# Kernel optimization log

Hardware: AMD Instinct MI355X
Metric: run time of the kernel (lower is better)

The kernel has to match this reference:

```python
import jax, jax.numpy as jnp
import numpy as np
import math

N, IN_DIM, OUT_DIM = 4096, 1024, 1024
MASK = True


def setup_inputs() -> dict:
    key = jax.random.key(0)
    ks = jax.random.split(key, 6)
    s = 1.0 / math.sqrt(IN_DIM)
    return {
        "qx": jax.random.normal(ks[0], (N, IN_DIM), jnp.float32),
        "kx": jax.random.normal(ks[1], (N, IN_DIM), jnp.float32),
        "vx": jax.random.normal(ks[2], (N, IN_DIM), jnp.float32),
        # torch nn.Linear weight layout: [out_dim, in_dim], y = x @ W.T
        "Wq": jax.random.normal(ks[3], (OUT_DIM, IN_DIM), jnp.float32) * s,
        "Wk": jax.random.normal(ks[4], (OUT_DIM, IN_DIM), jnp.float32) * s,
        "Wv": jax.random.normal(ks[5], (OUT_DIM, IN_DIM), jnp.float32) * s,
    }


def reference(qx, kx, vx, Wq, Wk, Wv):
    q = qx @ Wq.T  # [n, d]
    k = kx @ Wk.T
    v = vx @ Wv.T
    scores = (q @ k.T) / jnp.float32(math.sqrt(OUT_DIM))  # [n, n]
    if MASK:
        n = qx.shape[0]
        col = jnp.arange(n)[None, :]
        row = jnp.arange(n)[:, None]
        # original: -10000 where j > i (strictly upper triangular)
        scores = scores + jnp.where(col > row, jnp.float32(-10000.0), jnp.float32(0.0))
    attn = jax.nn.softmax(scores, axis=1)
    return attn @ v
```

## Files before the change

### kernel.cpp

```cpp
#include <hip/hip_runtime.h>
#include <hip/hip_bf16.h>
#include <stdint.h>

#define NTOK 4096
#define DIM  1024

typedef unsigned short u16;
typedef __bf16 bf16x8 __attribute__((ext_vector_type(8)));
typedef float f32x4 __attribute__((ext_vector_type(4)));
typedef u16 u16x8 __attribute__((ext_vector_type(8)));

__device__ __forceinline__ u16 f2bf(float f) {
  union { float f; uint32_t u; } c; c.f = f;
  return (u16)((c.u + 0x7fffu + ((c.u >> 16) & 1u)) >> 16);
}
__device__ __forceinline__ float bf2f(u16 b) {
  union { uint32_t u; float f; } c; c.u = (uint32_t)b << 16;
  return c.f;
}

__device__ __forceinline__ float wave_max(float v) {
#pragma unroll
  for (int o = 32; o; o >>= 1) v = fmaxf(v, __shfl_xor(v, o, 64));
  return v;
}
__device__ __forceinline__ float wave_sum(float v) {
#pragma unroll
  for (int o = 32; o; o >>= 1) v += __shfl_xor(v, o, 64);
  return v;
}

__device__ __forceinline__ int xcd_swz(int orig, int nwg) {
  const int q = nwg >> 3, r = nwg & 7;
  const int x = orig & 7, i = orig >> 3;
  return (x < r ? x * (q + 1) : r * (q + 1) + (x - r) * q) + i;
}

__device__ __forceinline__ void gld16(const u16* g, u16* l) {
  __builtin_amdgcn_global_load_lds((const __attribute__((address_space(1))) void*)g,
                                   (__attribute__((address_space(3))) void*)l, 16, 0, 0);
}

template<int N> __device__ __forceinline__ void wait_vmcnt() {
  if constexpr (N == 0) asm volatile("s_waitcnt vmcnt(0)" ::: "memory");
  else if constexpr (N == 6) asm volatile("s_waitcnt vmcnt(6)" ::: "memory");
  else if constexpr (N == 8) asm volatile("s_waitcnt vmcnt(8)" ::: "memory");
}

#define SFENCE() __builtin_amdgcn_sched_barrier(0)
#define BARF()   do { SFENCE(); __builtin_amdgcn_s_barrier(); SFENCE(); } while (0)
#define LGKM0F() do { SFENCE(); asm volatile("s_waitcnt lgkmcnt(0)" ::: "memory"); SFENCE(); } while (0)
#define VMC6F()  do { SFENCE(); asm volatile("s_waitcnt vmcnt(6)" ::: "memory"); SFENCE(); } while (0)
#define VMC0F()  do { SFENCE(); asm volatile("s_waitcnt vmcnt(0)" ::: "memory"); SFENCE(); } while (0)

__global__ __launch_bounds__(256) void cvt6(
    const float* __restrict__ qx, const float* __restrict__ kx, const float* __restrict__ vx,
    const float* __restrict__ Wq, const float* __restrict__ Wk, const float* __restrict__ Wv,
    u16* __restrict__ qxb, u16* __restrict__ kxb, u16* __restrict__ vxb,
    u16* __restrict__ Wqb, u16* __restrict__ Wkb, u16* __restrict__ Wvb,
    float* __restrict__ outZero)
{
  const int z = blockIdx.z;
  const int i = (blockIdx.x * 256 + threadIdx.x) * 8;
  if (z == 6) {
    if (i >= 2048 * DIM) return;
    const float4 zz = {0.f, 0.f, 0.f, 0.f};
    *reinterpret_cast<float4*>(outZero + i) = zz;
    *reinterpret_cast<float4*>(outZero + i + 4) = zz;
    return;
  }
  const int nelem = (z < 3) ? NTOK * DIM : DIM * DIM;
  if (i >= nelem) return;
  const float* in = (z == 0) ? qx : (z == 1) ? kx : (z == 2) ? vx
                  : (z == 3) ? Wq : (z == 4) ? Wk : Wv;
  u16* out = (z == 0) ? qxb : (z == 1) ? kxb : (z == 2) ? vxb
           : (z == 3) ? Wqb : (z == 4) ? Wkb : Wvb;
  float4 a = *reinterpret_cast<const float4*>(in + i);
  float4 b = *reinterpret_cast<const float4*>(in + i + 4);
  u16x8 o;
  o[0] = f2bf(a.x); o[1] = f2bf(a.y); o[2] = f2bf(a.z); o[3] = f2bf(a.w);
  o[4] = f2bf(b.x); o[5] = f2bf(b.y); o[6] = f2bf(b.z); o[7] = f2bf(b.w);
  *reinterpret_cast<u16x8*>(out + i) = o;
}

__device__ __forceinline__ void mm256(
    const u16* __restrict__ A, const u16* __restrict__ B,
    int lda, int ldb, int row0, int col0, int nt,
    u16* lds, f32x4 (&acc)[8][4])
{
  const int tid = threadIdx.x;
  const int wv = tid >> 6, lane = tid & 63;
  const int wm = wv >> 2, wn = wv & 3;
  const int l15 = lane & 15, l4 = lane >> 4;
  const int r8 = lane >> 3;
  const int gch = ((lane & 7) ^ r8) << 3;

  const int aStrip = wv >> 2;
  const int aSub   = (wv & 3) * 16;
  const int bStrip = wv >> 1;
  const int bSub   = (wv & 1) * 16;

  auto stageA = [&](int parity, int mh, int kt) {
    const int kofs = kt << 6;
#pragma unroll
    for (int jj = 0; jj < 2; ++jj) {
      const int rr = aSub + jj * 8;
      const int grow = row0 + aStrip * 128 + mh * 64 + rr + r8;
      u16* d = lds + parity * 32768 + mh * 8192 + aStrip * 4096 + rr * 64;
      gld16(A + (size_t)grow * lda + gch + kofs, d);
    }
  };
  auto stageB = [&](int parity, int nh, int kt) {
    const int kofs = kt << 6;
#pragma unroll
    for (int jj = 0; jj < 2; ++jj) {
      const int rr = bSub + jj * 8;
      const int grow = col0 + bStrip * 64 + nh * 32 + rr + r8;
      u16* d = lds + parity * 32768 + 16384 + nh * 8192 + bStrip * 2048 + rr * 64;
      gld16(B + (size_t)grow * ldb + gch + kofs, d);
    }
  };

  bf16x8 af[4][2];
  bf16x8 bfr[2][2][2];

  auto read_af = [&](int parity, int mh) {
#pragma unroll
    for (int mf = 0; mf < 4; ++mf)
#pragma unroll
      for (int ks = 0; ks < 2; ++ks) {
        const int rr = mf * 16 + l15;
        af[mf][ks] = *reinterpret_cast<const bf16x8*>(
            lds + parity * 32768 + mh * 8192 + wm * 4096 + rr * 64 +
            ((((ks << 2) + l4) ^ (rr & 7)) << 3));
      }
  };
  auto read_bf = [&](int parity, int nh) {
#pragma unroll
    for (int nf = 0; nf < 2; ++nf)
#pragma unroll
      for (int ks = 0; ks < 2; ++ks) {
        const int rr = nf * 16 + l15;
        bfr[nh][nf][ks] = *reinterpret_cast<const bf16x8*>(
            lds + parity * 32768 + 16384 + nh * 8192 + wn * 2048 + rr * 64 +
            ((((ks << 2) + l4) ^ (rr & 7)) << 3));
      }
  };
  auto quad = [&](int mh, int nh) {
    __builtin_amdgcn_s_setprio(1);
#pragma unroll
    for (int mf = 0; mf < 4; ++mf)
#pragma unroll
      for (int nf = 0; nf < 2; ++nf)
#pragma unroll
        for (int ks = 0; ks < 2; ++ks)
          acc[mh * 4 + mf][nh * 2 + nf] = __builtin_amdgcn_mfma_f32_16x16x32_bf16(
              af[mf][ks], bfr[nh][nf][ks], acc[mh * 4 + mf][nh * 2 + nf], 0, 0, 0);
    __builtin_amdgcn_s_setprio(0);
  };

  stageA(0, 0, 0); SFENCE();
  stageA(0, 1, 0); SFENCE();
  stageB(0, 0, 0); SFENCE();
  stageB(0, 1, 0); SFENCE();
  const int t1 = (nt > 1) ? 1 : 0;
  stageA(1, 0, t1); SFENCE();
  stageB(1, 0, t1); SFENCE();
  stageB(1, 1, t1); SFENCE();
  VMC0F();
  BARF();

  for (int t = 0; t < nt; ++t) {
    const int par = t & 1, nxt = par ^ 1;
    const int tp1 = (t + 1 < nt) ? t + 1 : nt - 1;
    const int tp2 = (t + 2 < nt) ? t + 2 : nt - 1;
    read_af(par, 0); read_bf(par, 0);
    stageA(nxt, 1, tp1);
    BARF(); LGKM0F();
    quad(0, 0);
    BARF();
    read_bf(par, 1);
    stageA(par, 0, tp2);
    BARF(); LGKM0F();
    quad(0, 1);
    BARF();
    read_af(par, 1);
    stageB(par, 0, tp2);
    BARF(); LGKM0F();
    quad(1, 0);
    BARF();
    stageB(par, 1, tp2);
    VMC6F();
    BARF();
    quad(1, 1);
    BARF();
  }

  VMC0F();
}

__global__ __launch_bounds__(512, 2) void proj256(
    const u16* __restrict__ qxb, const u16* __restrict__ kxb, const u16* __restrict__ vxb,
    const u16* __restrict__ Wqb, const u16* __restrict__ Wkb, const u16* __restrict__ Wvb,
    u16* __restrict__ qb, u16* __restrict__ kb, u16* __restrict__ vT)
{
  __shared__ alignas(16) u16 lds[65536];
  const int w = xcd_swz(blockIdx.x, 192);
  const int z = w >> 6, rem = w & 63;
  const int by = rem >> 2, bx = rem & 3;
  const u16* A = (z == 0) ? qxb : (z == 1) ? kxb : vxb;
  const u16* B = (z == 0) ? Wqb : (z == 1) ? Wkb : Wvb;
  const int row0 = by * 256, col0 = bx * 256;

  f32x4 acc[8][4] = {};
  mm256(A, B, DIM, DIM, row0, col0, DIM / 64, lds, acc);

  const int wv = threadIdx.x >> 6, lane = threadIdx.x & 63;
  const int wm = wv >> 2, wn = wv & 3;
  const int l15 = lane & 15, l4 = lane >> 4;
  const int om = row0 + wm * 128;
  const int on = col0 + wn * 64;
  if (z < 2) {
    u16* C = (z == 0) ? qb : kb;
#pragma unroll
    for (int m = 0; m < 8; ++m)
#pragma unroll
      for (int n = 0; n < 4; ++n)
#pragma unroll
        for (int r = 0; r < 4; ++r)
          C[(size_t)(om + m * 16 + l4 * 4 + r) * DIM + (on + n * 16 + l15)] = f2bf(acc[m][n][r]);
  } else {
#pragma unroll
    for (int m = 0; m < 8; ++m)
#pragma unroll
      for (int n = 0; n < 4; ++n) {
        ushort4 o;
        o.x = f2bf(acc[m][n][0]); o.y = f2bf(acc[m][n][1]);
        o.z = f2bf(acc[m][n][2]); o.w = f2bf(acc[m][n][3]);
        *reinterpret_cast<ushort4*>(&vT[(size_t)(on + n * 16 + l15) * NTOK + (om + m * 16 + l4 * 4)]) = o;
      }
  }
}

__global__ __launch_bounds__(512, 2) void scores256(
    const u16* __restrict__ A, const u16* __restrict__ B, u16* __restrict__ C, float scale)
{
  __shared__ alignas(16) u16 lds[65536];
  const int t = xcd_swz(blockIdx.x, 136);
  int by = (int)((sqrtf(8.0f * t + 1.0f) - 1.0f) * 0.5f);
  while ((by + 1) * (by + 2) / 2 <= t) ++by;
  while (by * (by + 1) / 2 > t) --by;
  const int bx = t - by * (by + 1) / 2;
  const int row0 = by * 256, col0 = bx * 256;

  f32x4 acc[8][4] = {};
  mm256(A, B, DIM, DIM, row0, col0, DIM / 64, lds, acc);

  const int wv = threadIdx.x >> 6, lane = threadIdx.x & 63;
  const int wm = wv >> 2, wn = wv & 3;
  const int l15 = lane & 15, l4 = lane >> 4;
  const int om = row0 + wm * 128;
  const int on = col0 + wn * 64;
#pragma unroll
  for (int m = 0; m < 8; ++m)
#pragma unroll
    for (int n = 0; n < 4; ++n)
#pragma unroll
      for (int r = 0; r < 4; ++r)
        C[(size_t)(om + m * 16 + l4 * 4 + r) * NTOK + (on + n * 16 + l15)] = f2bf(acc[m][n][r] * scale);
}

__device__ __forceinline__ void mm64(
    const u16* __restrict__ A, const u16* __restrict__ B,
    int lda, int ldb, int klo, int khi, int row0, int col0,
    u16* sA, u16* sB, f32x4 (&acc)[2][4])
{
  constexpr int ASZ = 64 * 64, BSZ = 128 * 64;
  const int tid = threadIdx.x;
  const int wave = tid >> 6, lane = tid & 63;
  const int wr = wave >> 1, wc = wave & 1;
  const int l15 = lane & 15, l4 = lane >> 4;
  const int h = l15 & 7;

  const int srow = lane >> 3;
  const int scol = ((lane & 7) ^ (lane >> 3)) << 3;
  const u16* gA = A + (size_t)(row0 + wave * 16 + srow) * lda + scol;
  const u16* gB = B + (size_t)(col0 + wave * 32 + srow) * ldb + scol;
  const int lbA = wave * 16 * 64;
  const int lbB = wave * 32 * 64;

  auto stage = [&](int k0, u16* bA, u16* bB) {
#pragma unroll
    for (int i = 0; i < 2; ++i)
      gld16(gA + (size_t)(i * 8) * lda + k0, bA + lbA + i * 512);
#pragma unroll
    for (int i = 0; i < 4; ++i)
      gld16(gB + (size_t)(i * 8) * ldb + k0, bB + lbB + i * 512);
  };

  stage(klo, sA, sB);
  int cur = 0;
  for (int k0 = klo; k0 < khi; k0 += 64) {
    const bool more = (k0 + 64 < khi);
    if (more) {
      stage(k0 + 64, sA + (cur ^ 1) * ASZ, sB + (cur ^ 1) * BSZ);
      SFENCE(); wait_vmcnt<6>(); SFENCE();
    } else {
      SFENCE(); wait_vmcnt<0>(); SFENCE();
    }
    __builtin_amdgcn_s_barrier();
    SFENCE();

    const char* bA = (const char*)(sA + cur * ASZ);
    const char* bB = (const char*)(sB + cur * BSZ);
#pragma unroll
    for (int ks = 0; ks < 2; ++ks) {
      bf16x8 af[2], bfv[4];
#pragma unroll
      for (int mf = 0; mf < 2; ++mf)
        af[mf] = *reinterpret_cast<const bf16x8*>(
            bA + ((wr * 32 + mf * 16 + l15) << 7) + ((((ks << 2) + l4) ^ h) << 4));
#pragma unroll
      for (int nf = 0; nf < 4; ++nf)
        bfv[nf] = *reinterpret_cast<const bf16x8*>(
            bB + ((wc * 64 + nf * 16 + l15) << 7) + ((((ks << 2) + l4) ^ h) << 4));
#pragma unroll
      for (int mf = 0; mf < 2; ++mf)
#pragma unroll
        for (int nf = 0; nf < 4; ++nf)
          acc[mf][nf] = __builtin_amdgcn_mfma_f32_16x16x32_bf16(af[mf], bfv[nf], acc[mf][nf], 0, 0, 0);
    }

    SFENCE();
    __builtin_amdgcn_s_barrier();
    SFENCE();
    cur ^= 1;
  }
}

__global__ __launch_bounds__(256) void gemm_pv(
    const u16* __restrict__ P, const u16* __restrict__ vT, float* __restrict__ C)
{
  __shared__ alignas(16) u16 sA[2 * 64 * 64];
  __shared__ alignas(16) u16 sB[2 * 128 * 64];
  const int w = xcd_swz(blockIdx.x, 768);
  const int bx = w & 7;
  const int cid = w >> 3;
  int by, half;
  if (cid < 32) { by = cid; half = -1; }
  else { const int j = cid - 32; by = 32 + (j >> 1); half = j & 1; }
  const int row0 = by * 64, col0 = bx * 128;
  const int Klim = row0 + 64;
  int klo = 0, khi = Klim;
  if (half >= 0) {
    const int h1 = (((Klim >> 6) + 1) >> 1) << 6;
    if (half == 0) khi = h1; else klo = h1;
  }

  f32x4 acc[2][4] = {};
  mm64(P, vT, NTOK, NTOK, klo, khi, row0, col0, sA, sB, acc);

  const int lane = threadIdx.x & 63;
  const int wave = threadIdx.x >> 6;
  const int l15 = lane & 15, l4 = lane >> 4;
  const int om = row0 + (wave >> 1) * 32;
  const int on = col0 + (wave & 1) * 64;
#pragma unroll
  for (int mf = 0; mf < 2; ++mf)
#pragma unroll
    for (int nf = 0; nf < 4; ++nf)
#pragma unroll
      for (int r = 0; r < 4; ++r) {
        const size_t idx = (size_t)(om + mf * 16 + l4 * 4 + r) * DIM + (on + nf * 16 + l15);
        if (half >= 0) atomicAdd(&C[idx], acc[mf][nf][r]);
        else C[idx] = acc[mf][nf][r];
      }
}

__global__ __launch_bounds__(256) void softmax_causal(const u16* __restrict__ S,
                                                      u16* __restrict__ P) {
  __shared__ float buf[NTOK];
  __shared__ float red[8];
  const int row = blockIdx.x;
  const int tid = threadIdx.x;
  const int limit = row + 1;
  const int limit128 = (row & ~127) + 128;
  const u16* srow = S + (size_t)row * NTOK;

  float lmax = -1e30f;
  for (int j = tid * 8; j < limit128; j += 2048) {
    float v[8];
    if (j + 8 <= limit) {
      u16x8 sv = *reinterpret_cast<const u16x8*>(srow + j);
#pragma unroll
      for (int e = 0; e < 8; ++e) v[e] = bf2f(sv[e]);
    } else {
#pragma unroll
      for (int e = 0; e < 8; ++e) v[e] = (j + e < limit) ? bf2f(srow[j + e]) : -1e30f;
    }
    float4 lo = {v[0], v[1], v[2], v[3]}, hi = {v[4], v[5], v[6], v[7]};
    *reinterpret_cast<float4*>(buf + j) = lo;
    *reinterpret_cast<float4*>(buf + j + 4) = hi;
#pragma unroll
    for (int e = 0; e < 8; ++e) lmax = fmaxf(lmax, v[e]);
  }
  lmax = wave_max(lmax);
  if ((tid & 63) == 0) red[tid >> 6] = lmax;
  __syncthreads();
  const float m = fmaxf(fmaxf(red[0], red[1]), fmaxf(red[2], red[3]));

  float lsum = 0.f;
  for (int j = tid * 8; j < limit128; j += 2048) {
    float4 lo = *reinterpret_cast<float4*>(buf + j);
    float4 hi = *reinterpret_cast<float4*>(buf + j + 4);
    float e0 = __expf(lo.x - m), e1 = __expf(lo.y - m), e2 = __expf(lo.z - m), e3 = __expf(lo.w - m);
    float e4 = __expf(hi.x - m), e5 = __expf(hi.y - m), e6 = __expf(hi.z - m), e7 = __expf(hi.w - m);
    float4 eo = {e0, e1, e2, e3}, eh = {e4, e5, e6, e7};
    *reinterpret_cast<float4*>(buf + j) = eo;
    *reinterpret_cast<float4*>(buf + j + 4) = eh;
    lsum += ((e0 + e1) + (e2 + e3)) + ((e4 + e5) + (e6 + e7));
  }
  lsum = wave_sum(lsum);
  if ((tid & 63) == 0) red[4 + (tid >> 6)] = lsum;
  __syncthreads();
  const float inv = 1.0f / (red[4] + red[5] + red[6] + red[7]);

  u16* prow = P + (size_t)row * NTOK;
  for (int j = tid * 8; j < limit128; j += 2048) {
    float4 lo = *reinterpret_cast<float4*>(buf + j);
    float4 hi = *reinterpret_cast<float4*>(buf + j + 4);
    u16x8 o;
    o[0] = f2bf(lo.x * inv); o[1] = f2bf(lo.y * inv);
    o[2] = f2bf(lo.z * inv); o[3] = f2bf(lo.w * inv);
    o[4] = f2bf(hi.x * inv); o[5] = f2bf(hi.y * inv);
    o[6] = f2bf(hi.z * inv); o[7] = f2bf(hi.w * inv);
    *reinterpret_cast<u16x8*>(prow + j) = o;
  }
}

extern "C" void kernel_launch(void* const* d_in, const int* in_sizes, int n_in,
                              void* d_out, int out_size, void* d_ws, size_t ws_size,
                              hipStream_t stream) {
  const float* qx = (const float*)d_in[0];
  const float* kx = (const float*)d_in[1];
  const float* vx = (const float*)d_in[2];
  const float* Wq = (const float*)d_in[3];
  const float* Wk = (const float*)d_in[4];
  const float* Wv = (const float*)d_in[5];
  float* out = (float*)d_out;
  char* ws = (char*)d_ws;
  const size_t MB = 1024ull * 1024ull;

  if (ws_size < 120 * MB) {
    hipMemsetAsync(d_out, 0xFF, (size_t)out_size * sizeof(float), stream);
    return;
  }

  u16* qxb = (u16*)(ws);
  u16* kxb = (u16*)(ws + 8 * MB);
  u16* vxb = (u16*)(ws + 16 * MB);
  u16* Wqb = (u16*)(ws + 24 * MB);
  u16* Wkb = (u16*)(ws + 26 * MB);
  u16* Wvb = (u16*)(ws + 28 * MB);
  u16* S   = (u16*)(ws);
  u16* qb  = (u16*)(ws + 64 * MB);
  u16* kb  = (u16*)(ws + 72 * MB);
  u16* vT  = (u16*)(ws + 80 * MB);
  u16* P   = (u16*)(ws + 88 * MB);

  cvt6<<<dim3(NTOK * DIM / (256 * 8), 1, 7), 256, 0, stream>>>(
      qx, kx, vx, Wq, Wk, Wv, qxb, kxb, vxb, Wqb, Wkb, Wvb,
      out + (size_t)2048 * DIM);

  proj256<<<192, 512, 0, stream>>>(qxb, kxb, vxb, Wqb, Wkb, Wvb, qb, kb, vT);

  scores256<<<136, 512, 0, stream>>>(qb, kb, S, 0.03125f);

  softmax_causal<<<NTOK, 256, 0, stream>>>(S, P);

  gemm_pv<<<768, 256, 0, stream>>>(P, vT, out);
}
```

Measured before the change: 127.5 us.

## Loosen scheduling fences in GEMM loop and widen softmax blocks to 512

Removes most sched_barrier fences around barriers and staging calls in the pipelined GEMM mainloop, so the compiler can interleave LDS reads, global-to-LDS loads and MFMAs more freely. Separately, the causal softmax kernel moves from 256 to 512 threads per row, so each row is covered in a single pass and the reductions span eight waves. The risk is that the compiler reorders waits or MFMAs in ways that hurt the hand-tuned pipeline, and that short early rows leave many softmax threads idle.

Result: slower. 131.0 us (+2.8%).

```diff
diff --git a/kernel.cpp b/kernel.cpp
--- a/kernel.cpp
+++ b/kernel.cpp
@@ -48,8 +48,8 @@
 }
 
 #define SFENCE() __builtin_amdgcn_sched_barrier(0)
-#define BARF()   do { SFENCE(); __builtin_amdgcn_s_barrier(); SFENCE(); } while (0)
-#define LGKM0F() do { SFENCE(); asm volatile("s_waitcnt lgkmcnt(0)" ::: "memory"); SFENCE(); } while (0)
+#define BAR()    __builtin_amdgcn_s_barrier()
+#define LGKM0F() do { asm volatile("s_waitcnt lgkmcnt(0)" ::: "memory"); SFENCE(); } while (0)
 #define VMC6F()  do { SFENCE(); asm volatile("s_waitcnt vmcnt(6)" ::: "memory"); SFENCE(); } while (0)
 #define VMC0F()  do { SFENCE(); asm volatile("s_waitcnt vmcnt(0)" ::: "memory"); SFENCE(); } while (0)
 
@@ -159,16 +159,11 @@
     __builtin_amdgcn_s_setprio(0);
   };
 
-  stageA(0, 0, 0); SFENCE();
-  stageA(0, 1, 0); SFENCE();
-  stageB(0, 0, 0); SFENCE();
-  stageB(0, 1, 0); SFENCE();
+  stageA(0, 0, 0); stageA(0, 1, 0); stageB(0, 0, 0); stageB(0, 1, 0);
   const int t1 = (nt > 1) ? 1 : 0;
-  stageA(1, 0, t1); SFENCE();
-  stageB(1, 0, t1); SFENCE();
-  stageB(1, 1, t1); SFENCE();
+  stageA(1, 0, t1); stageB(1, 0, t1); stageB(1, 1, t1);
   VMC0F();
-  BARF();
+  BAR();
 
   for (int t = 0; t < nt; ++t) {
     const int par = t & 1, nxt = par ^ 1;
@@ -176,24 +171,24 @@
     const int tp2 = (t + 2 < nt) ? t + 2 : nt - 1;
     read_af(par, 0); read_bf(par, 0);
     stageA(nxt, 1, tp1);
-    BARF(); LGKM0F();
+    BAR(); LGKM0F();
     quad(0, 0);
-    BARF();
+    BAR();
     read_bf(par, 1);
     stageA(par, 0, tp2);
-    BARF(); LGKM0F();
+    BAR(); LGKM0F();
     quad(0, 1);
-    BARF();
+    BAR();
     read_af(par, 1);
     stageB(par, 0, tp2);
-    BARF(); LGKM0F();
+    BAR(); LGKM0F();
     quad(1, 0);
-    BARF();
+    BAR();
     stageB(par, 1, tp2);
     VMC6F();
-    BARF();
+    BAR();
     quad(1, 1);
-    BARF();
+    BAR();
   }
 
   VMC0F();
@@ -377,18 +372,19 @@
       }
 }
 
-__global__ __launch_bounds__(256) void softmax_causal(const u16* __restrict__ S,
+__global__ __launch_bounds__(512) void softmax_causal(const u16* __restrict__ S,
                                                       u16* __restrict__ P) {
   __shared__ float buf[NTOK];
-  __shared__ float red[8];
+  __shared__ float red[16];
   const int row = blockIdx.x;
   const int tid = threadIdx.x;
+  const int wid = tid >> 6;
   const int limit = row + 1;
   const int limit128 = (row & ~127) + 128;
   const u16* srow = S + (size_t)row * NTOK;
 
   float lmax = -1e30f;
-  for (int j = tid * 8; j < limit128; j += 2048) {
+  for (int j = tid * 8; j < limit128; j += 4096) {
     float v[8];
     if (j + 8 <= limit) {
       u16x8 sv = *reinterpret_cast<const u16x8*>(srow + j);
@@ -405,12 +401,14 @@
     for (int e = 0; e < 8; ++e) lmax = fmaxf(lmax, v[e]);
   }
   lmax = wave_max(lmax);
-  if ((tid & 63) == 0) red[tid >> 6] = lmax;
+  if ((tid & 63) == 0) red[wid] = lmax;
   __syncthreads();
-  const float m = fmaxf(fmaxf(red[0], red[1]), fmaxf(red[2], red[3]));
+  float m = red[0];
+#pragma unroll
+  for (int i = 1; i < 8; ++i) m = fmaxf(m, red[i]);
 
   float lsum = 0.f;
-  for (int j = tid * 8; j < limit128; j += 2048) {
+  for (int j = tid * 8; j < limit128; j += 4096) {
     float4 lo = *reinterpret_cast<float4*>(buf + j);
     float4 hi = *reinterpret_cast<float4*>(buf + j + 4);
     float e0 = __expf(lo.x - m), e1 = __expf(lo.y - m), e2 = __expf(lo.z - m), e3 = __expf(lo.w - m);
@@ -421,12 +419,15 @@
     lsum += ((e0 + e1) + (e2 + e3)) + ((e4 + e5) + (e6 + e7));
   }
   lsum = wave_sum(lsum);
-  if ((tid & 63) == 0) red[4 + (tid >> 6)] = lsum;
+  if ((tid & 63) == 0) red[8 + wid] = lsum;
   __syncthreads();
-  const float inv = 1.0f / (red[4] + red[5] + red[6] + red[7]);
+  float s = red[8];
+#pragma unroll
+  for (int i = 1; i < 8; ++i) s += red[8 + i];
+  const float inv = 1.0f / s;
 
   u16* prow = P + (size_t)row * NTOK;
-  for (int j = tid * 8; j < limit128; j += 2048) {
+  for (int j = tid * 8; j < limit128; j += 4096) {
     float4 lo = *reinterpret_cast<float4*>(buf + j);
     float4 hi = *reinterpret_cast<float4*>(buf + j + 4);
     u16x8 o;
@@ -476,7 +477,7 @@
 
   scores256<<<136, 512, 0, stream>>>(qb, kb, S, 0.03125f);
 
-  softmax_causal<<<NTOK, 256, 0, stream>>>(S, P);
+  softmax_causal<<<NTOK, 512, 0, stream>>>(S, P);
 
   gemm_pv<<<768, 256, 0, stream>>>(P, vT, out);
 }
```
